# Kernel optimization log

Measured on AMD Instinct MI355X. Metric: run time of the kernel, lower is better.

Reference implementation:

```python
import jax, jax.numpy as jnp
import numpy as np

N = 50000
E = 500000
STRUCT = 128
SEM = 768
HID = 128
HEADS = 4


def setup_inputs() -> dict:
    key = jax.random.key(0)
    ks = jax.random.split(key, 16)
    rn = lambda k, s, sc=0.05: jax.random.normal(k, s, dtype=jnp.float32) * sc
    in_dim = STRUCT + SEM
    return {
        "x": rn(ks[0], (N, in_dim), 1.0),
        "edge_index": jax.random.randint(ks[1], (2, E), 0, N),
        "Wq": rn(ks[2], (STRUCT, HID)),
        "Wk": rn(ks[3], (SEM, HID)),
        "Wv": rn(ks[4], (SEM, HID)),
        "Wo": rn(ks[5], (STRUCT + HID, STRUCT)),
        "bo": jnp.zeros((STRUCT,), jnp.float32),
        "W1": rn(ks[6], (in_dim, HEADS * HID)),
        "att_src1": rn(ks[7], (HEADS, HID)),
        "att_dst1": rn(ks[8], (HEADS, HID)),
        "b1": jnp.zeros((HEADS * HID,), jnp.float32),
        "g1_w": jnp.ones((HEADS * HID,), jnp.float32),
        "g1_b": jnp.zeros((HEADS * HID,), jnp.float32),
        "g1_ms": jnp.ones((HEADS * HID,), jnp.float32),
        "W2": rn(ks[9], (HEADS * HID, HID)),
        "att_src2": rn(ks[10], (1, HID)),
        "att_dst2": rn(ks[11], (1, HID)),
        "b2": jnp.zeros((HID,), jnp.float32),
        "g2_w": jnp.ones((HID,), jnp.float32),
        "g2_b": jnp.zeros((HID,), jnp.float32),
        "g2_ms": jnp.ones((HID,), jnp.float32),
        "Wn": rn(ks[12], (HID, 2)),
        "bn": jnp.zeros((2,), jnp.float32),
    }


def gat_conv(x, src, dst, W, att_src, att_dst, bias, heads, out_c, concat):
    # PyG GATConv (self loops already appended to src/dst by caller)
    n = x.shape[0]
    h = (x @ W).reshape(n, heads, out_c)              # [N,H,C]
    a_src = (h * att_src).sum(-1)                      # [N,H]
    a_dst = (h * att_dst).sum(-1)                      # [N,H]
    alpha = jax.nn.leaky_relu(a_src[src] + a_dst[dst], 0.2)  # [Etot,H]
    amax = jax.ops.segment_max(alpha, dst, num_segments=n)
    amax = jnp.where(jnp.isfinite(amax), amax, 0.0)
    ex = jnp.exp(alpha - amax[dst])
    denom = jax.ops.segment_sum(ex, dst, num_segments=n)
    att = ex / (denom[dst] + 1e-16)                    # segment softmax over dst
    msg = h[src] * att[:, :, None]                     # [Etot,H,C]
    out = jax.ops.segment_sum(msg, dst, num_segments=n)
    out = out.reshape(n, heads * out_c) if concat else out.mean(1)
    return out + bias


def graph_norm(x, weight, bias, mean_scale, eps=1e-5):
    mean = x.mean(0, keepdims=True)
    out = x - mean * mean_scale
    var = (out * out).mean(0, keepdims=True)
    return out / jnp.sqrt(var + eps) * weight + bias


def reference(x, edge_index, Wq, Wk, Wv, Wo, bo, W1, att_src1, att_dst1, b1,
              g1_w, g1_b, g1_ms, W2, att_src2, att_dst2, b2, g2_w, g2_b, g2_ms,
              Wn, bn):
    x_struct = x[:, :STRUCT]
    x_sem = x[:, STRUCT:]
    # CrossModalFusion
    Q = x_struct @ Wq
    K = x_sem @ Wk
    V = x_sem @ Wv
    scores = (Q * K).sum(-1, keepdims=True)
    attn = jax.nn.sigmoid(scores) * V
    h0 = jnp.concatenate([x_struct, attn], axis=1) @ Wo + bo
    h = jnp.concatenate([h0, x_sem], axis=1)
    # add self loops once
    n = x.shape[0]
    loop = jnp.arange(n, dtype=edge_index.dtype)
    src = jnp.concatenate([edge_index[0], loop])
    dst = jnp.concatenate([edge_index[1], loop])
    h = gat_conv(h, src, dst, W1, att_src1, att_dst1, b1, HEADS, HID, True)
    h = jax.nn.elu(graph_norm(h, g1_w, g1_b, g1_ms))
    h = gat_conv(h, src, dst, W2, att_src2, att_dst2, b2, 1, HID, False)
    h = jax.nn.elu(graph_norm(h, g2_w, g2_b, g2_ms))
    return h @ Wn + bn
```

## Files before the change

### kernel.cpp

```cpp
#include <hip/hip_runtime.h>
#include <math.h>

#define NN 50000
#define NE 500000
#define EEDG 550000
#define SDIM 128
#define MDIM 768
#define HIDD 128
#define NHEADS 4
#define INDIM 896
#define H1D 512
#define SCAN_NB 196
#define MP 50048
#define MT 391

typedef unsigned short u16;
typedef unsigned int u32;
typedef __attribute__((ext_vector_type(8))) short short8;
typedef __attribute__((ext_vector_type(4))) float f32x4;

__device__ __forceinline__ u16 f2bf(float f) {
    union { float f; u32 u; } v; v.f = f;
    u32 r = v.u + 0x7FFFu + ((v.u >> 16) & 1u);
    return (u16)(r >> 16);
}
__device__ __forceinline__ float bf2f(u16 h) {
    union { u32 u; float f; } v; v.u = ((u32)h) << 16;
    return v.f;
}

__device__ __forceinline__ void gl_lds16(const u16* g, u16* l) {
    __builtin_amdgcn_global_load_lds(
        (const __attribute__((address_space(1))) void*)g,
        (__attribute__((address_space(3))) void*)l, 16, 0, 0);
}

__device__ __forceinline__ void edge_sd(const int* __restrict__ ei, int e, int& s, int& d) {
    if (e < NE) { s = ei[e]; d = ei[NE + e]; }
    else        { s = e - NE; d = e - NE; }
}

__global__ __launch_bounds__(256) void cast_weights(
    const float* __restrict__ Wq, const float* __restrict__ Wk, const float* __restrict__ Wv,
    const float* __restrict__ Wo, const float* __restrict__ W1, const float* __restrict__ W2,
    u16* __restrict__ wqT, u16* __restrict__ wkT, u16* __restrict__ wvT,
    u16* __restrict__ woT, u16* __restrict__ w1T, u16* __restrict__ w2T,
    int* __restrict__ degcur, float* __restrict__ msum)
{
    const int SQ = 128 * 128, SK = 128 * 768, SV = 128 * 768,
              SO = 256 * 128, S1 = 896 * 512, S2 = 512 * 128;
    long i = (long)blockIdx.x * 256 + threadIdx.x;
    long w = i;
    if (w < SQ) { int n = (int)(w / 128), k = (int)(w % 128); wqT[w] = f2bf(Wq[(size_t)k * 128 + n]); return; }
    w -= SQ;
    if (w < SK) { int n = (int)(w / 768), k = (int)(w % 768); wkT[w] = f2bf(Wk[(size_t)k * 128 + n]); return; }
    w -= SK;
    if (w < SV) { int n = (int)(w / 768), k = (int)(w % 768); wvT[w] = f2bf(Wv[(size_t)k * 128 + n]); return; }
    w -= SV;
    if (w < SO) { int n = (int)(w / 256), k = (int)(w % 256); woT[w] = f2bf(Wo[(size_t)k * 128 + n]); return; }
    w -= SO;
    if (w < S1) { int n = (int)(w / 896), k = (int)(w % 896); w1T[w] = f2bf(W1[(size_t)k * 512 + n]); return; }
    w -= S1;
    if (w < S2) { int n = (int)(w / 512), k = (int)(w % 512); w2T[w] = f2bf(W2[(size_t)k * 128 + n]); return; }
    w -= S2;
    if (w < 2 * NN) { degcur[w] = 0; return; }
    w -= 2 * NN;
    if (w < 1024) msum[w] = 0.f;
}

__global__ __launch_bounds__(256) void cast_pad_x(const float4* __restrict__ x4, u16* __restrict__ xb) {
    const long total = (long)MP * 224;
    long i = (long)blockIdx.x * blockDim.x + threadIdx.x;
    long stride = (long)gridDim.x * blockDim.x;
    for (; i < total; i += stride) {
        int row = (int)(i / 224);
        int c4 = (int)(i - (long)row * 224);
        float4 v = make_float4(0.f, 0.f, 0.f, 0.f);
        if (row < NN) v = x4[(size_t)row * 224 + c4];
        short4 o;
        o.x = (short)f2bf(v.x); o.y = (short)f2bf(v.y);
        o.z = (short)f2bf(v.z); o.w = (short)f2bf(v.w);
        *(short4*)(xb + (size_t)row * 896 + c4 * 4) = o;
    }
}

__global__ __launch_bounds__(256) void count_deg(const int* __restrict__ ei, int* __restrict__ deg) {
    int e = blockIdx.x * 256 + threadIdx.x;
    if (e >= EEDG) return;
    int d = e < NE ? ei[NE + e] : e - NE;
    atomicAdd(&deg[d], 1);
}

__global__ __launch_bounds__(256) void scan_bsum(const int* __restrict__ deg, int* __restrict__ part) {
    __shared__ int s[256];
    int t = threadIdx.x;
    int idx = blockIdx.x * 256 + t;
    s[t] = idx < NN ? deg[idx] : 0;
    __syncthreads();
    for (int off = 128; off; off >>= 1) {
        if (t < off) s[t] += s[t + off];
        __syncthreads();
    }
    if (t == 0) part[blockIdx.x] = s[0];
}

__global__ __launch_bounds__(256) void scan_part(int* __restrict__ part) {
    __shared__ int s[256];
    int t = threadIdx.x;
    int v = t < SCAN_NB ? part[t] : 0;
    s[t] = v;
    __syncthreads();
    for (int off = 1; off < 256; off <<= 1) {
        int x = t >= off ? s[t - off] : 0;
        __syncthreads();
        s[t] += x;
        __syncthreads();
    }
    if (t < SCAN_NB) part[t] = s[t] - v;
}

__global__ __launch_bounds__(256) void scan_write(const int* __restrict__ deg, const int* __restrict__ part,
                                                  int* __restrict__ rowptr) {
    __shared__ int s[256];
    int t = threadIdx.x;
    int idx = blockIdx.x * 256 + t;
    int v = idx < NN ? deg[idx] : 0;
    s[t] = v;
    __syncthreads();
    for (int off = 1; off < 256; off <<= 1) {
        int x = t >= off ? s[t - off] : 0;
        __syncthreads();
        s[t] += x;
        __syncthreads();
    }
    if (idx < NN) rowptr[idx] = part[blockIdx.x] + s[t] - v;
    if (idx == NN - 1) rowptr[NN] = EEDG;
}

__global__ __launch_bounds__(256) void fill_csr(const int* __restrict__ ei, const int* __restrict__ rowptr,
                                                int* __restrict__ cur, int* __restrict__ esrc,
                                                int* __restrict__ edst) {
    int e = blockIdx.x * 256 + threadIdx.x;
    if (e >= EEDG) return;
    int s, d;
    edge_sd(ei, e, s, d);
    int p = rowptr[d] + atomicAdd(&cur[d], 1);
    esrc[p] = s;
    edst[p] = d;
}

template<int H>
__global__ __launch_bounds__(256) void edge_exp(const int* __restrict__ esrc, const int* __restrict__ edst,
    const float* __restrict__ asrc, const float* __restrict__ adst, float* __restrict__ exf)
{
    int i = blockIdx.x * 256 + threadIdx.x;
    if (i >= EEDG) return;
    int s = esrc[i], d = edst[i];
    if (H == 4) {
        float4 as = *(const float4*)(asrc + s * 4);
        float4 ad = *(const float4*)(adst + d * 4);
        float4 o;
        float a;
        a = as.x + ad.x; a = a >= 0.f ? a : 0.2f * a; o.x = expf(a);
        a = as.y + ad.y; a = a >= 0.f ? a : 0.2f * a; o.y = expf(a);
        a = as.z + ad.z; a = a >= 0.f ? a : 0.2f * a; o.z = expf(a);
        a = as.w + ad.w; a = a >= 0.f ? a : 0.2f * a; o.w = expf(a);
        *(float4*)(exf + (size_t)i * 4) = o;
    } else {
        float a = asrc[s] + adst[d];
        a = a >= 0.f ? a : 0.2f * a;
        exf[i] = expf(a);
    }
}

template<int OUT_BF16, int DOTS, int DH>
__device__ __forceinline__ void gemm_body(
    u16* __restrict__ Asm, u16* __restrict__ Bsm,
    const u16* __restrict__ A1, int lda1, int K1,
    const u16* __restrict__ A2, int lda2, int K2,
    const u16* __restrict__ Bw,
    void* __restrict__ Cout, int ldc,
    const float* __restrict__ bias, int row0, int col0,
    const float* __restrict__ dvs, const float* __restrict__ dvd,
    float* __restrict__ aout_s, float* __restrict__ aout_d)
{
    const int tid = threadIdx.x;
    const int wave = tid >> 6, lane = tid & 63;
    const int wr = wave >> 1, wc = wave & 1;
    const int K = K1 + K2;
    const int srow = tid >> 2;
    const int skp = (tid & 3) * 8;
    const int l15 = lane & 15, l4 = lane >> 4;

    f32x4 acc[4][4];
    #pragma unroll
    for (int i = 0; i < 4; ++i)
        #pragma unroll
        for (int j = 0; j < 4; ++j)
            acc[i][j] = (f32x4){0.f, 0.f, 0.f, 0.f};

    for (int k0 = 0; k0 < K; k0 += 32) {
        const u16* Ab; int la; int kk;
        if (k0 < K1) { Ab = A1; la = lda1; kk = k0; }
        else         { Ab = A2; la = lda2; kk = k0 - K1; }
        gl_lds16(Ab + (size_t)(row0 + srow) * la + kk + skp,      Asm + srow * 32 + skp);
        gl_lds16(Ab + (size_t)(row0 + srow + 64) * la + kk + skp, Asm + (srow + 64) * 32 + skp);
        gl_lds16(Bw + (size_t)(col0 + srow) * K + k0 + skp,       Bsm + srow * 32 + skp);
        gl_lds16(Bw + (size_t)(col0 + srow + 64) * K + k0 + skp,  Bsm + (srow + 64) * 32 + skp);
        __syncthreads();
        short8 af[4], bfr[4];
        #pragma unroll
        for (int m = 0; m < 4; ++m)
            af[m] = *(const short8*)(Asm + (wr * 64 + m * 16 + l15) * 32 + l4 * 8);
        #pragma unroll
        for (int n = 0; n < 4; ++n)
            bfr[n] = *(const short8*)(Bsm + (wc * 64 + n * 16 + l15) * 32 + l4 * 8);
        #pragma unroll
        for (int m = 0; m < 4; ++m)
            #pragma unroll
            for (int n = 0; n < 4; ++n)
                acc[m][n] = __builtin_amdgcn_mfma_f32_16x16x32_bf16(af[m], bfr[n], acc[m][n], 0, 0, 0);
        __syncthreads();
    }
    #pragma unroll
    for (int m = 0; m < 4; ++m) {
        int r = row0 + wr * 64 + m * 16 + l4 * 4;
        #pragma unroll
        for (int n = 0; n < 4; ++n) {
            int c = col0 + wc * 64 + n * 16 + l15;
            float bv = bias ? bias[c] : 0.f;
            #pragma unroll
            for (int q = 0; q < 4; ++q) {
                float v = acc[m][n][q] + bv;
                if (OUT_BF16) ((u16*)Cout)[(size_t)(r + q) * ldc + c] = f2bf(v);
                else          ((float*)Cout)[(size_t)(r + q) * ldc + c] = v;
            }
        }
    }
    if (DOTS) {
        const int head = (DH == 1) ? 0 : (col0 >> 7);
        const float* svp = dvs + head * 128;
        const float* dvp = dvd + head * 128;
        float sv[4], dv[4];
        #pragma unroll
        for (int n = 0; n < 4; ++n) {
            int cc = wc * 64 + n * 16 + l15;
            sv[n] = svp[cc];
            dv[n] = dvp[cc];
        }
        __shared__ float red[128][2][2];
        #pragma unroll
        for (int m = 0; m < 4; ++m) {
            #pragma unroll
            for (int q = 0; q < 4; ++q) {
                float ps = 0.f, pd = 0.f;
                #pragma unroll
                for (int n = 0; n < 4; ++n) {
                    ps = fmaf(acc[m][n][q], sv[n], ps);
                    pd = fmaf(acc[m][n][q], dv[n], pd);
                }
                #pragma unroll
                for (int off = 1; off < 16; off <<= 1) {
                    ps += __shfl_xor(ps, off);
                    pd += __shfl_xor(pd, off);
                }
                if (l15 == 0) {
                    int lr = wr * 64 + m * 16 + l4 * 4 + q;
                    red[lr][wc][0] = ps;
                    red[lr][wc][1] = pd;
                }
            }
        }
        __syncthreads();
        if (tid < 128) {
            int r = row0 + tid;
            aout_s[(size_t)r * DH + head] = red[tid][0][0] + red[tid][1][0];
            aout_d[(size_t)r * DH + head] = red[tid][0][1] + red[tid][1][1];
        }
    }
}

template<int OUT_BF16, int DOTS, int DH>
__global__ __launch_bounds__(256) void gemm_mfma(
    const u16* __restrict__ A1, int lda1, int K1,
    const u16* __restrict__ A2, int lda2, int K2,
    const u16* __restrict__ Bw,
    void* __restrict__ Cout, int ldc,
    const float* __restrict__ bias,
    const float* __restrict__ dvs, const float* __restrict__ dvd,
    float* __restrict__ aout_s, float* __restrict__ aout_d)
{
    __shared__ u16 Asm[128 * 32];
    __shared__ u16 Bsm[128 * 32];
    gemm_body<OUT_BF16, DOTS, DH>(Asm, Bsm, A1, lda1, K1, A2, lda2, K2, Bw, Cout, ldc, bias,
                                  blockIdx.y * 128, blockIdx.x * 128, dvs, dvd, aout_s, aout_d);
}

__global__ __launch_bounds__(256) void gemm_w1(
    const u16* __restrict__ A1, const u16* __restrict__ A2,
    const u16* __restrict__ Bw, u16* __restrict__ Cout)
{
    __shared__ u16 Asm[128 * 32];
    __shared__ u16 Bsm[128 * 32];
    const int nwg = 4 * MT;
    const int q = nwg / 8, r = nwg % 8;
    int orig = blockIdx.x;
    int xcd = orig & 7;
    int lg = (xcd < r ? xcd * (q + 1) : r * (q + 1) + (xcd - r) * q) + (orig >> 3);
    int col0 = (lg & 3) * 128;
    int row0 = (lg >> 2) * 128;
    gemm_body<1, 0, 1>(Asm, Bsm, A1, 128, 128, A2, 896, 768, Bw, Cout, 512, nullptr,
                       row0, col0, nullptr, nullptr, nullptr, nullptr);
}

__global__ __launch_bounds__(256) void gemm_qkv(
    const u16* __restrict__ xb,
    const u16* __restrict__ wqT, const u16* __restrict__ wkT, const u16* __restrict__ wvT,
    u16* __restrict__ qb, u16* __restrict__ kb, u16* __restrict__ vb)
{
    __shared__ u16 Asm[128 * 32];
    __shared__ u16 Bsm[128 * 32];
    const u16* A; const u16* B; int K; u16* C;
    if (blockIdx.x == 0)      { A = xb;       B = wqT; K = 128; C = qb; }
    else if (blockIdx.x == 1) { A = xb + 128; B = wkT; K = 768; C = kb; }
    else                      { A = xb + 128; B = wvT; K = 768; C = vb; }
    gemm_body<1, 0, 1>(Asm, Bsm, A, 896, K, (const u16*)nullptr, 0, 0, B, C, 128, nullptr,
                       blockIdx.y * 128, 0, nullptr, nullptr, nullptr, nullptr);
}

__global__ __launch_bounds__(128) void node_attn_b(const u16* __restrict__ Q,
                                                   const u16* __restrict__ K,
                                                   u16* __restrict__ V)
{
    int nd = blockIdx.x;
    int t = threadIdx.x;
    size_t base = (size_t)nd * HIDD;
    float p = bf2f(Q[base + t]) * bf2f(K[base + t]);
    #pragma unroll
    for (int off = 32; off; off >>= 1) p += __shfl_down(p, off);
    __shared__ float sm[2];
    if ((t & 63) == 0) sm[t >> 6] = p;
    __syncthreads();
    float s = sm[0] + sm[1];
    float sig = 1.f / (1.f + expf(-s));
    V[base + t] = f2bf(bf2f(V[base + t]) * sig);
}

__global__ __launch_bounds__(256) void att_dots1_b(const u16* __restrict__ h1,
    const float* __restrict__ asv, const float* __restrict__ adv,
    float* __restrict__ a_src, float* __restrict__ a_dst)
{
    int nd = blockIdx.x;
    int t = threadIdx.x;
    int w = t >> 6, l = t & 63;
    const u16* hr = h1 + (size_t)nd * H1D + w * HIDD;
    const float* sv = asv + w * HIDD;
    const float* dv = adv + w * HIDD;
    float h0v = bf2f(hr[l]), h1v = bf2f(hr[l + 64]);
    float ps = h0v * sv[l] + h1v * sv[l + 64];
    float pd = h0v * dv[l] + h1v * dv[l + 64];
    #pragma unroll
    for (int off = 32; off; off >>= 1) {
        ps += __shfl_down(ps, off);
        pd += __shfl_down(pd, off);
    }
    if (l == 0) { a_src[nd * NHEADS + w] = ps; a_dst[nd * NHEADS + w] = pd; }
}

#define ACC4(P, AA) { \
    n0 = fmaf(bf2f((u16)(P).x), AA, n0); \
    n1 = fmaf(bf2f((u16)((P).x >> 16)), AA, n1); \
    n2 = fmaf(bf2f((u16)(P).y), AA, n2); \
    n3 = fmaf(bf2f((u16)((P).y >> 16)), AA, n3); }

__global__ __launch_bounds__(128) void agg1_f(const int* __restrict__ rowptr, const int* __restrict__ esrc,
    const float* __restrict__ exf,
    const u16* __restrict__ h1b, const float* __restrict__ bias, u16* __restrict__ o1b)
{
    int d = blockIdx.x;
    int t = threadIdx.x;
    int c0 = t * 4;
    int h = t >> 5;
    int beg = rowptr[d], end = rowptr[d + 1];
    float n0 = 0.f, n1 = 0.f, n2 = 0.f, n3 = 0.f, den = 0.f;
    int i = beg;
    for (; i + 7 < end; i += 8) {
        int s0 = esrc[i], s1 = esrc[i+1], s2 = esrc[i+2], s3 = esrc[i+3];
        int s4 = esrc[i+4], s5 = esrc[i+5], s6 = esrc[i+6], s7 = esrc[i+7];
        float a0 = exf[(size_t)i*4+h],     a1 = exf[(size_t)(i+1)*4+h];
        float a2 = exf[(size_t)(i+2)*4+h], a3 = exf[(size_t)(i+3)*4+h];
        float a4 = exf[(size_t)(i+4)*4+h], a5 = exf[(size_t)(i+5)*4+h];
        float a6 = exf[(size_t)(i+6)*4+h], a7 = exf[(size_t)(i+7)*4+h];
        uint2 p0 = *(const uint2*)(h1b + (size_t)s0 * H1D + c0);
        uint2 p1 = *(const uint2*)(h1b + (size_t)s1 * H1D + c0);
        uint2 p2 = *(const uint2*)(h1b + (size_t)s2 * H1D + c0);
        uint2 p3 = *(const uint2*)(h1b + (size_t)s3 * H1D + c0);
        uint2 p4 = *(const uint2*)(h1b + (size_t)s4 * H1D + c0);
        uint2 p5 = *(const uint2*)(h1b + (size_t)s5 * H1D + c0);
        uint2 p6 = *(const uint2*)(h1b + (size_t)s6 * H1D + c0);
        uint2 p7 = *(const uint2*)(h1b + (size_t)s7 * H1D + c0);
        den += ((a0 + a1) + (a2 + a3)) + ((a4 + a5) + (a6 + a7));
        ACC4(p0, a0) ACC4(p1, a1) ACC4(p2, a2) ACC4(p3, a3)
        ACC4(p4, a4) ACC4(p5, a5) ACC4(p6, a6) ACC4(p7, a7)
    }
    for (; i < end; ++i) {
        int sA = esrc[i];
        float aA = exf[(size_t)i * 4 + h];
        uint2 pA = *(const uint2*)(h1b + (size_t)sA * H1D + c0);
        den += aA;
        ACC4(pA, aA)
    }
    float invd = 1.f / (den + 1e-16f);
    float4 bv = *(const float4*)(bias + c0);
    u32 o0 = (u32)f2bf(n0 * invd + bv.x) | ((u32)f2bf(n1 * invd + bv.y) << 16);
    u32 o1 = (u32)f2bf(n2 * invd + bv.z) | ((u32)f2bf(n3 * invd + bv.w) << 16);
    *(uint2*)(o1b + (size_t)d * H1D + c0) = make_uint2(o0, o1);
}

__global__ __launch_bounds__(256) void agg2_f(const int* __restrict__ rowptr, const int* __restrict__ esrc,
    const float* __restrict__ exf,
    const u16* __restrict__ h2b, const float* __restrict__ bias, float* __restrict__ o2,
    float* __restrict__ msum)
{
    if (blockIdx.x == 0) {
        msum[threadIdx.x] = 0.f;
        msum[threadIdx.x + 256] = 0.f;
        msum[threadIdx.x + 512] = 0.f;
        msum[threadIdx.x + 768] = 0.f;
    }
    int w = threadIdx.x >> 6, l = threadIdx.x & 63;
    int d = blockIdx.x * 4 + w;
    if (d >= NN) return;
    int c0 = l * 2;
    int beg = rowptr[d], end = rowptr[d + 1];
    float n0 = 0.f, n1 = 0.f, den = 0.f;
    int i = beg;
    for (; i + 7 < end; i += 8) {
        int s0 = esrc[i], s1 = esrc[i+1], s2 = esrc[i+2], s3 = esrc[i+3];
        int s4 = esrc[i+4], s5 = esrc[i+5], s6 = esrc[i+6], s7 = esrc[i+7];
        float a0 = exf[i],   a1 = exf[i+1], a2 = exf[i+2], a3 = exf[i+3];
        float a4 = exf[i+4], a5 = exf[i+5], a6 = exf[i+6], a7 = exf[i+7];
        u32 p0 = *(const u32*)(h2b + (size_t)s0 * HIDD + c0);
        u32 p1 = *(const u32*)(h2b + (size_t)s1 * HIDD + c0);
        u32 p2 = *(const u32*)(h2b + (size_t)s2 * HIDD + c0);
        u32 p3 = *(const u32*)(h2b + (size_t)s3 * HIDD + c0);
        u32 p4 = *(const u32*)(h2b + (size_t)s4 * HIDD + c0);
        u32 p5 = *(const u32*)(h2b + (size_t)s5 * HIDD + c0);
        u32 p6 = *(const u32*)(h2b + (size_t)s6 * HIDD + c0);
        u32 p7 = *(const u32*)(h2b + (size_t)s7 * HIDD + c0);
        den += ((a0 + a1) + (a2 + a3)) + ((a4 + a5) + (a6 + a7));
        n0 = fmaf(bf2f((u16)p0), a0, n0); n1 = fmaf(bf2f((u16)(p0 >> 16)), a0, n1);
        n0 = fmaf(bf2f((u16)p1), a1, n0); n1 = fmaf(bf2f((u16)(p1 >> 16)), a1, n1);
        n0 = fmaf(bf2f((u16)p2), a2, n0); n1 = fmaf(bf2f((u16)(p2 >> 16)), a2, n1);
        n0 = fmaf(bf2f((u16)p3), a3, n0); n1 = fmaf(bf2f((u16)(p3 >> 16)), a3, n1);
        n0 = fmaf(bf2f((u16)p4), a4, n0); n1 = fmaf(bf2f((u16)(p4 >> 16)), a4, n1);
        n0 = fmaf(bf2f((u16)p5), a5, n0); n1 = fmaf(bf2f((u16)(p5 >> 16)), a5, n1);
        n0 = fmaf(bf2f((u16)p6), a6, n0); n1 = fmaf(bf2f((u16)(p6 >> 16)), a6, n1);
        n0 = fmaf(bf2f((u16)p7), a7, n0); n1 = fmaf(bf2f((u16)(p7 >> 16)), a7, n1);
    }
    for (; i < end; ++i) {
        int sA = esrc[i];
        float aA = exf[i];
        u32 pA = *(const u32*)(h2b + (size_t)sA * HIDD + c0);
        den += aA;
        n0 = fmaf(bf2f((u16)pA), aA, n0);
        n1 = fmaf(bf2f((u16)(pA >> 16)), aA, n1);
    }
    float invd = 1.f / (den + 1e-16f);
    o2[(size_t)d * HIDD + c0]     = n0 * invd + bias[c0];
    o2[(size_t)d * HIDD + c0 + 1] = n1 * invd + bias[c0 + 1];
}

__global__ void colstat_b(const u16* __restrict__ x, float* __restrict__ msum,
                          float* __restrict__ vsum, int n, int rpb)
{
    int C = blockDim.x;
    int c = threadIdx.x;
    int r0 = blockIdx.x * rpb;
    int r1 = min(n, r0 + rpb);
    float s = 0.f, s2 = 0.f;
    for (int r = r0; r < r1; ++r) {
        float v = bf2f(x[(size_t)r * C + c]);
        s += v;
        s2 += v * v;
    }
    atomicAdd(&msum[c], s);
    atomicAdd(&vsum[c], s2);
}

__global__ void apply_norm_elu_b(u16* __restrict__ x, const float* __restrict__ msum,
                                 const float* __restrict__ vsum, const float* __restrict__ ms,
                                 const float* __restrict__ w, const float* __restrict__ b,
                                 int n, int rpb)
{
    int C = blockDim.x;
    int c = threadIdx.x;
    const float invn = 1.f / (float)NN;
    float mean = msum[c] * invn;
    float sub = mean * ms[c];
    float var = vsum[c] * invn - 2.f * sub * mean + sub * sub;
    float inv = rsqrtf(var + 1e-5f);
    float wc = w[c] * inv, bc = b[c];
    int r0 = blockIdx.x * rpb;
    int r1 = min(n, r0 + rpb);
    for (int r = r0; r < r1; ++r) {
        float v = (bf2f(x[(size_t)r * C + c]) - sub) * wc + bc;
        v = v > 0.f ? v : expm1f(v);
        x[(size_t)r * C + c] = f2bf(v);
    }
}

__global__ void colstat(const float* __restrict__ x, float* __restrict__ msum,
                        float* __restrict__ vsum, int n, int rpb)
{
    int C = blockDim.x;
    int c = threadIdx.x;
    int r0 = blockIdx.x * rpb;
    int r1 = min(n, r0 + rpb);
    float s = 0.f, s2 = 0.f;
    for (int r = r0; r < r1; ++r) {
        float v = x[(size_t)r * C + c];
        s += v;
        s2 += v * v;
    }
    atomicAdd(&msum[c], s);
    atomicAdd(&vsum[c], s2);
}

__global__ __launch_bounds__(128) void norm2_proj(const float* __restrict__ o2,
    const float* __restrict__ msum, const float* __restrict__ vsum,
    const float* __restrict__ ms, const float* __restrict__ w, const float* __restrict__ b,
    const float* __restrict__ Wn, const float* __restrict__ bn, float* __restrict__ out)
{
    int nd = blockIdx.x;
    int t = threadIdx.x;
    const float invn = 1.f / (float)NN;
    float mean = msum[t] * invn;
    float sub = mean * ms[t];
    float var = vsum[t] * invn - 2.f * sub * mean + sub * sub;
    float inv = rsqrtf(var + 1e-5f);
    float v = (o2[(size_t)nd * HIDD + t] - sub) * w[t] * inv + b[t];
    v = v > 0.f ? v : expm1f(v);
    float p0 = v * Wn[t * 2], p1 = v * Wn[t * 2 + 1];
    #pragma unroll
    for (int off = 32; off; off >>= 1) {
        p0 += __shfl_down(p0, off);
        p1 += __shfl_down(p1, off);
    }
    __shared__ float sm[4];
    if ((t & 63) == 0) { sm[t >> 6] = p0; sm[2 + (t >> 6)] = p1; }
    __syncthreads();
    if (t == 0) {
        out[nd * 2 + 0] = sm[0] + sm[1] + bn[0];
        out[nd * 2 + 1] = sm[2] + sm[3] + bn[1];
    }
}

extern "C" void kernel_launch(void* const* d_in, const int* in_sizes, int n_in,
                              void* d_out, int out_size, void* d_ws, size_t ws_size,
                              hipStream_t stream)
{
    const float* x   = (const float*)d_in[0];
    const int*   ei  = (const int*)d_in[1];
    const float* Wq  = (const float*)d_in[2];
    const float* Wk  = (const float*)d_in[3];
    const float* Wv  = (const float*)d_in[4];
    const float* Wo  = (const float*)d_in[5];
    const float* bo  = (const float*)d_in[6];
    const float* W1  = (const float*)d_in[7];
    const float* as1 = (const float*)d_in[8];
    const float* ad1 = (const float*)d_in[9];
    const float* b1  = (const float*)d_in[10];
    const float* g1w = (const float*)d_in[11];
    const float* g1b = (const float*)d_in[12];
    const float* g1m = (const float*)d_in[13];
    const float* W2  = (const float*)d_in[14];
    const float* as2 = (const float*)d_in[15];
    const float* ad2 = (const float*)d_in[16];
    const float* b2  = (const float*)d_in[17];
    const float* g2w = (const float*)d_in[18];
    const float* g2b = (const float*)d_in[19];
    const float* g2m = (const float*)d_in[20];
    const float* Wn  = (const float*)d_in[21];
    const float* bn  = (const float*)d_in[22];
    float* out = (float*)d_out;

    u16* usw = (u16*)d_ws;
    size_t uo = 0;
    u16* xb  = usw + uo; uo += (size_t)MP * 896;
    u16* h1b = usw + uo; uo += (size_t)MP * 512;
    u16* qb  = usw + uo; uo += (size_t)MP * 128;
    u16* kb  = usw + uo; uo += (size_t)MP * 128;
    u16* vb  = usw + uo; uo += (size_t)MP * 128;
    u16* o1b = usw + uo; uo += (size_t)MP * 512;
    u16* wqT = usw + uo; uo += 128 * 128;
    u16* wkT = usw + uo; uo += 128 * 768;
    u16* wvT = usw + uo; uo += 128 * 768;
    u16* woT = usw + uo; uo += 128 * 256;
    u16* w1T = usw + uo; uo += 512 * 896;
    u16* w2T = usw + uo; uo += 128 * 512;
    float* fws = (float*)(usw + uo);
    size_t fo = 0;
    float* asrc = fws + fo; fo += (size_t)MP * NHEADS;
    float* adst = fws + fo; fo += (size_t)MP * NHEADS;
    float* exf  = fws + fo; fo += (size_t)EEDG * NHEADS;
    float* msum = fws + fo; fo += 512;
    float* vsum = fws + fo; fo += 512;
    int* iws = (int*)(fws + fo);
    size_t io = 0;
    int* rowptr = iws + io; io += NN + 1;
    int* degcur = iws + io; io += 2 * NN;
    int* esrc   = iws + io; io += EEDG;
    int* edst   = iws + io; io += EEDG;
    int* spart  = iws + io; io += 256;
    int* cur    = degcur + NN;
    float* o2  = (float*)xb;
    u16* h0b = qb;
    u16* h2b = kb;

    const int EB = (EEDG + 255) / 256;
    const int CW_BLOCKS = (770048 + 2 * NN + 1024 + 255) / 256;

    cast_weights<<<CW_BLOCKS, 256, 0, stream>>>(Wq, Wk, Wv, Wo, W1, W2,
                                                wqT, wkT, wvT, woT, w1T, w2T,
                                                degcur, msum);
    cast_pad_x<<<8192, 256, 0, stream>>>((const float4*)x, xb);

    count_deg<<<EB, 256, 0, stream>>>(ei, degcur);
    scan_bsum<<<SCAN_NB, 256, 0, stream>>>(degcur, spart);
    scan_part<<<1, 256, 0, stream>>>(spart);
    scan_write<<<SCAN_NB, 256, 0, stream>>>(degcur, spart, rowptr);
    fill_csr<<<EB, 256, 0, stream>>>(ei, rowptr, cur, esrc, edst);

    gemm_qkv<<<dim3(3, MT), 256, 0, stream>>>(xb, wqT, wkT, wvT, qb, kb, vb);
    node_attn_b<<<NN, 128, 0, stream>>>(qb, kb, vb);

    gemm_mfma<1, 0, 1><<<dim3(1, MT), 256, 0, stream>>>(xb, 896, 128, vb, 128, 128, woT, h0b, 128, bo,
                                                        nullptr, nullptr, nullptr, nullptr);

    gemm_w1<<<4 * MT, 256, 0, stream>>>(h0b, xb + 128, w1T, h1b);

    att_dots1_b<<<NN, 256, 0, stream>>>(h1b, as1, ad1, asrc, adst);
    edge_exp<NHEADS><<<EB, 256, 0, stream>>>(esrc, edst, asrc, adst, exf);
    agg1_f<<<NN, 128, 0, stream>>>(rowptr, esrc, exf, h1b, b1, o1b);

    colstat_b<<<(NN + 127) / 128, H1D, 0, stream>>>(o1b, msum, vsum, NN, 128);
    apply_norm_elu_b<<<(NN + 127) / 128, H1D, 0, stream>>>(o1b, msum, vsum, g1m, g1w, g1b, NN, 128);

    gemm_mfma<1, 1, 1><<<dim3(1, MT), 256, 0, stream>>>(o1b, 512, 512, (const u16*)nullptr, 0, 0, w2T, h2b, 128,
                                                        nullptr, as2, ad2, asrc, adst);
    edge_exp<1><<<EB, 256, 0, stream>>>(esrc, edst, asrc, adst, exf);
    agg2_f<<<(NN + 3) / 4, 256, 0, stream>>>(rowptr, esrc, exf, h2b, b2, o2, msum);

    colstat<<<(NN + 127) / 128, HIDD, 0, stream>>>(o2, msum, vsum, NN, 128);
    norm2_proj<<<NN, 128, 0, stream>>>(o2, msum, vsum, g2m, g2w, g2b, Wn, bn, out);
}
```

Baseline: 608.4 us.

## Merge independent prep kernels and fuse layer-1 column stats into aggregation

Degree counting is merged into the x-cast launch, and CSR fill is merged into the QKV GEMM launch as extra blocks. This removes launches and lets independent work overlap. The separate colstat pass over o1b is removed: agg1_f now accumulates column sums and squared sums with atomics into 32 partitioned buffers, and the normalization kernel reduces those partitions. This saves a full read of the 50000x512 activation, but adds 4M float atomics with contention across 32 partitions.

```diff
diff --git a/kernel.cpp b/kernel.cpp
--- a/kernel.cpp
+++ b/kernel.cpp
@@ -13,6 +13,8 @@
 #define SCAN_NB 196
 #define MP 50048
 #define MT 391
+#define EB 2149
+#define NPART 32
 
 typedef unsigned short u16;
 typedef unsigned int u32;
@@ -65,13 +67,22 @@
     w -= S2;
     if (w < 2 * NN) { degcur[w] = 0; return; }
     w -= 2 * NN;
-    if (w < 1024) msum[w] = 0.f;
-}
-
-__global__ __launch_bounds__(256) void cast_pad_x(const float4* __restrict__ x4, u16* __restrict__ xb) {
+    if (w < 1024 + 2 * NPART * 512) msum[w] = 0.f;
+}
+
+__global__ __launch_bounds__(256) void prep2(const int* __restrict__ ei, int* __restrict__ deg,
+                                             const float4* __restrict__ x4, u16* __restrict__ xb)
+{
+    if (blockIdx.x < EB) {
+        int e = blockIdx.x * 256 + threadIdx.x;
+        if (e >= EEDG) return;
+        int d = e < NE ? ei[NE + e] : e - NE;
+        atomicAdd(&deg[d], 1);
+        return;
+    }
     const long total = (long)MP * 224;
-    long i = (long)blockIdx.x * blockDim.x + threadIdx.x;
-    long stride = (long)gridDim.x * blockDim.x;
+    long i = (long)(blockIdx.x - EB) * 256 + threadIdx.x;
+    long stride = (long)(gridDim.x - EB) * 256;
     for (; i < total; i += stride) {
         int row = (int)(i / 224);
         int c4 = (int)(i - (long)row * 224);
@@ -82,13 +93,6 @@
         o.z = (short)f2bf(v.z); o.w = (short)f2bf(v.w);
         *(short4*)(xb + (size_t)row * 896 + c4 * 4) = o;
     }
-}
-
-__global__ __launch_bounds__(256) void count_deg(const int* __restrict__ ei, int* __restrict__ deg) {
-    int e = blockIdx.x * 256 + threadIdx.x;
-    if (e >= EEDG) return;
-    int d = e < NE ? ei[NE + e] : e - NE;
-    atomicAdd(&deg[d], 1);
 }
 
 __global__ __launch_bounds__(256) void scan_bsum(const int* __restrict__ deg, int* __restrict__ part) {
@@ -135,18 +139,6 @@
     }
     if (idx < NN) rowptr[idx] = part[blockIdx.x] + s[t] - v;
     if (idx == NN - 1) rowptr[NN] = EEDG;
-}
-
-__global__ __launch_bounds__(256) void fill_csr(const int* __restrict__ ei, const int* __restrict__ rowptr,
-                                                int* __restrict__ cur, int* __restrict__ esrc,
-                                                int* __restrict__ edst) {
-    int e = blockIdx.x * 256 + threadIdx.x;
-    if (e >= EEDG) return;
-    int s, d;
-    edge_sd(ei, e, s, d);
-    int p = rowptr[d] + atomicAdd(&cur[d], 1);
-    esrc[p] = s;
-    edst[p] = d;
 }
 
 template<int H>
@@ -313,19 +305,34 @@
                        row0, col0, nullptr, nullptr, nullptr, nullptr);
 }
 
-__global__ __launch_bounds__(256) void gemm_qkv(
+__global__ __launch_bounds__(256) void gemm_qkv_fill(
     const u16* __restrict__ xb,
     const u16* __restrict__ wqT, const u16* __restrict__ wkT, const u16* __restrict__ wvT,
-    u16* __restrict__ qb, u16* __restrict__ kb, u16* __restrict__ vb)
+    u16* __restrict__ qb, u16* __restrict__ kb, u16* __restrict__ vb,
+    const int* __restrict__ ei, const int* __restrict__ rowptr,
+    int* __restrict__ cur, int* __restrict__ esrc, int* __restrict__ edst)
 {
     __shared__ u16 Asm[128 * 32];
     __shared__ u16 Bsm[128 * 32];
+    int bid = blockIdx.x;
+    if (bid >= 3 * MT) {
+        int e = (bid - 3 * MT) * 256 + threadIdx.x;
+        if (e >= EEDG) return;
+        int s, d;
+        edge_sd(ei, e, s, d);
+        int p = rowptr[d] + atomicAdd(&cur[d], 1);
+        esrc[p] = s;
+        edst[p] = d;
+        return;
+    }
+    int sel = bid / MT;
+    int row = bid - sel * MT;
     const u16* A; const u16* B; int K; u16* C;
-    if (blockIdx.x == 0)      { A = xb;       B = wqT; K = 128; C = qb; }
-    else if (blockIdx.x == 1) { A = xb + 128; B = wkT; K = 768; C = kb; }
-    else                      { A = xb + 128; B = wvT; K = 768; C = vb; }
+    if (sel == 0)      { A = xb;       B = wqT; K = 128; C = qb; }
+    else if (sel == 1) { A = xb + 128; B = wkT; K = 768; C = kb; }
+    else               { A = xb + 128; B = wvT; K = 768; C = vb; }
     gemm_body<1, 0, 1>(Asm, Bsm, A, 896, K, (const u16*)nullptr, 0, 0, B, C, 128, nullptr,
-                       blockIdx.y * 128, 0, nullptr, nullptr, nullptr, nullptr);
+                       row * 128, 0, nullptr, nullptr, nullptr, nullptr);
 }
 
 __global__ __launch_bounds__(128) void node_attn_b(const u16* __restrict__ Q,
@@ -375,7 +382,8 @@
 
 __global__ __launch_bounds__(128) void agg1_f(const int* __restrict__ rowptr, const int* __restrict__ esrc,
     const float* __restrict__ exf,
-    const u16* __restrict__ h1b, const float* __restrict__ bias, u16* __restrict__ o1b)
+    const u16* __restrict__ h1b, const float* __restrict__ bias, u16* __restrict__ o1b,
+    float* __restrict__ statm, float* __restrict__ statv)
 {
     int d = blockIdx.x;
     int t = threadIdx.x;
@@ -412,9 +420,19 @@
     }
     float invd = 1.f / (den + 1e-16f);
     float4 bv = *(const float4*)(bias + c0);
-    u32 o0 = (u32)f2bf(n0 * invd + bv.x) | ((u32)f2bf(n1 * invd + bv.y) << 16);
-    u32 o1 = (u32)f2bf(n2 * invd + bv.z) | ((u32)f2bf(n3 * invd + bv.w) << 16);
-    *(uint2*)(o1b + (size_t)d * H1D + c0) = make_uint2(o0, o1);
+    u16 q0 = f2bf(n0 * invd + bv.x);
+    u16 q1 = f2bf(n1 * invd + bv.y);
+    u16 q2 = f2bf(n2 * invd + bv.z);
+    u16 q3 = f2bf(n3 * invd + bv.w);
+    *(uint2*)(o1b + (size_t)d * H1D + c0) =
+        make_uint2((u32)q0 | ((u32)q1 << 16), (u32)q2 | ((u32)q3 << 16));
+    float r0 = bf2f(q0), r1 = bf2f(q1), r2 = bf2f(q2), r3 = bf2f(q3);
+    float* sm_ = statm + (d & (NPART - 1)) * 512 + c0;
+    float* sv_ = statv + (d & (NPART - 1)) * 512 + c0;
+    atomicAdd(sm_ + 0, r0); atomicAdd(sv_ + 0, r0 * r0);
+    atomicAdd(sm_ + 1, r1); atomicAdd(sv_ + 1, r1 * r1);
+    atomicAdd(sm_ + 2, r2); atomicAdd(sv_ + 2, r2 * r2);
+    atomicAdd(sm_ + 3, r3); atomicAdd(sv_ + 3, r3 * r3);
 }
 
 __global__ __launch_bounds__(256) void agg2_f(const int* __restrict__ rowptr, const int* __restrict__ esrc,
@@ -471,34 +489,23 @@
     o2[(size_t)d * HIDD + c0 + 1] = n1 * invd + bias[c0 + 1];
 }
 
-__global__ void colstat_b(const u16* __restrict__ x, float* __restrict__ msum,
-                          float* __restrict__ vsum, int n, int rpb)
+__global__ void apply_norm_elu_b(u16* __restrict__ x, const float* __restrict__ statm,
+                                 const float* __restrict__ statv, const float* __restrict__ ms,
+                                 const float* __restrict__ w, const float* __restrict__ b,
+                                 int n, int rpb)
 {
     int C = blockDim.x;
     int c = threadIdx.x;
-    int r0 = blockIdx.x * rpb;
-    int r1 = min(n, r0 + rpb);
-    float s = 0.f, s2 = 0.f;
-    for (int r = r0; r < r1; ++r) {
-        float v = bf2f(x[(size_t)r * C + c]);
-        s += v;
-        s2 += v * v;
-    }
-    atomicAdd(&msum[c], s);
-    atomicAdd(&vsum[c], s2);
-}
-
-__global__ void apply_norm_elu_b(u16* __restrict__ x, const float* __restrict__ msum,
-                                 const float* __restrict__ vsum, const float* __restrict__ ms,
-                                 const float* __restrict__ w, const float* __restrict__ b,
-                                 int n, int rpb)
-{
-    int C = blockDim.x;
-    int c = threadIdx.x;
+    float msum_ = 0.f, vsum_ = 0.f;
+    #pragma unroll
+    for (int p = 0; p < NPART; ++p) {
+        msum_ += statm[p * 512 + c];
+        vsum_ += statv[p * 512 + c];
+    }
     const float invn = 1.f / (float)NN;
-    float mean = msum[c] * invn;
+    float mean = msum_ * invn;
     float sub = mean * ms[c];
-    float var = vsum[c] * invn - 2.f * sub * mean + sub * sub;
+    float var = vsum_ * invn - 2.f * sub * mean + sub * sub;
     float inv = rsqrtf(var + 1e-5f);
     float wc = w[c] * inv, bc = b[c];
     int r0 = blockIdx.x * rpb;
@@ -606,6 +613,8 @@
     float* exf  = fws + fo; fo += (size_t)EEDG * NHEADS;
     float* msum = fws + fo; fo += 512;
     float* vsum = fws + fo; fo += 512;
+    float* statm = fws + fo; fo += NPART * 512;
+    float* statv = fws + fo; fo += NPART * 512;
     int* iws = (int*)(fws + fo);
     size_t io = 0;
     int* rowptr = iws + io; io += NN + 1;
@@ -618,21 +627,19 @@
     u16* h0b = qb;
     u16* h2b = kb;
 
-    const int EB = (EEDG + 255) / 256;
-    const int CW_BLOCKS = (770048 + 2 * NN + 1024 + 255) / 256;
+    const int CW_BLOCKS = (770048 + 2 * NN + 1024 + 2 * NPART * 512 + 255) / 256;
 
     cast_weights<<<CW_BLOCKS, 256, 0, stream>>>(Wq, Wk, Wv, Wo, W1, W2,
                                                 wqT, wkT, wvT, woT, w1T, w2T,
                                                 degcur, msum);
-    cast_pad_x<<<8192, 256, 0, stream>>>((const float4*)x, xb);
-
-    count_deg<<<EB, 256, 0, stream>>>(ei, degcur);
+    prep2<<<EB + 8192, 256, 0, stream>>>(ei, degcur, (const float4*)x, xb);
+
     scan_bsum<<<SCAN_NB, 256, 0, stream>>>(degcur, spart);
     scan_part<<<1, 256, 0, stream>>>(spart);
     scan_write<<<SCAN_NB, 256, 0, stream>>>(degcur, spart, rowptr);
-    fill_csr<<<EB, 256, 0, stream>>>(ei, rowptr, cur, esrc, edst);
-
-    gemm_qkv<<<dim3(3, MT), 256, 0, stream>>>(xb, wqT, wkT, wvT, qb, kb, vb);
+
+    gemm_qkv_fill<<<3 * MT + EB, 256, 0, stream>>>(xb, wqT, wkT, wvT, qb, kb, vb,
+                                                   ei, rowptr, cur, esrc, edst);
     node_attn_b<<<NN, 128, 0, stream>>>(qb, kb, vb);
 
     gemm_mfma<1, 0, 1><<<dim3(1, MT), 256, 0, stream>>>(xb, 896, 128, vb, 128, 128, woT, h0b, 128, bo,
@@ -642,10 +649,9 @@
 
     att_dots1_b<<<NN, 256, 0, stream>>>(h1b, as1, ad1, asrc, adst);
     edge_exp<NHEADS><<<EB, 256, 0, stream>>>(esrc, edst, asrc, adst, exf);
-    agg1_f<<<NN, 128, 0, stream>>>(rowptr, esrc, exf, h1b, b1, o1b);
-
-    colstat_b<<<(NN + 127) / 128, H1D, 0, stream>>>(o1b, msum, vsum, NN, 128);
-    apply_norm_elu_b<<<(NN + 127) / 128, H1D, 0, stream>>>(o1b, msum, vsum, g1m, g1w, g1b, NN, 128);
+    agg1_f<<<NN, 128, 0, stream>>>(rowptr, esrc, exf, h1b, b1, o1b, statm, statv);
+
+    apply_norm_elu_b<<<(NN + 127) / 128, H1D, 0, stream>>>(o1b, statm, statv, g1m, g1w, g1b, NN, 128);
 
     gemm_mfma<1, 1, 1><<<dim3(1, MT), 256, 0, stream>>>(o1b, 512, 512, (const u16*)nullptr, 0, 0, w2T, h2b, 128,
                                                         nullptr, as2, ad2, asrc, adst);
```

Measured after the change: 1.265 ms. 2.08x slower.

## Merge independent graph-prep kernels into GEMM/cast launches to overlap work

Applied to the files above, without the earlier changes.

Folds degree counting into the x-cast kernel and CSR fill into the QKV GEMM kernel using block-index partitioning, so independent graph-building work runs concurrently with dense work and two launches are removed. The QKV grid also changes from 2D (3 x MT) to 1D with a sel/row decode. This is meant to hide the small, latency-bound atomic kernels behind the larger bandwidth/compute kernels. The cost is that the fill blocks allocate unused LDS, and the mixed block types may unbalance scheduling.

```diff
diff --git a/kernel.cpp b/kernel.cpp
--- a/kernel.cpp
+++ b/kernel.cpp
@@ -13,6 +13,7 @@
 #define SCAN_NB 196
 #define MP 50048
 #define MT 391
+#define EB 2149
 
 typedef unsigned short u16;
 typedef unsigned int u32;
@@ -68,10 +69,19 @@
     if (w < 1024) msum[w] = 0.f;
 }
 
-__global__ __launch_bounds__(256) void cast_pad_x(const float4* __restrict__ x4, u16* __restrict__ xb) {
+__global__ __launch_bounds__(256) void prep2(const int* __restrict__ ei, int* __restrict__ deg,
+                                             const float4* __restrict__ x4, u16* __restrict__ xb)
+{
+    if (blockIdx.x < EB) {
+        int e = blockIdx.x * 256 + threadIdx.x;
+        if (e >= EEDG) return;
+        int d = e < NE ? ei[NE + e] : e - NE;
+        atomicAdd(&deg[d], 1);
+        return;
+    }
     const long total = (long)MP * 224;
-    long i = (long)blockIdx.x * blockDim.x + threadIdx.x;
-    long stride = (long)gridDim.x * blockDim.x;
+    long i = (long)(blockIdx.x - EB) * 256 + threadIdx.x;
+    long stride = (long)(gridDim.x - EB) * 256;
     for (; i < total; i += stride) {
         int row = (int)(i / 224);
         int c4 = (int)(i - (long)row * 224);
@@ -82,13 +92,6 @@
         o.z = (short)f2bf(v.z); o.w = (short)f2bf(v.w);
         *(short4*)(xb + (size_t)row * 896 + c4 * 4) = o;
     }
-}
-
-__global__ __launch_bounds__(256) void count_deg(const int* __restrict__ ei, int* __restrict__ deg) {
-    int e = blockIdx.x * 256 + threadIdx.x;
-    if (e >= EEDG) return;
-    int d = e < NE ? ei[NE + e] : e - NE;
-    atomicAdd(&deg[d], 1);
 }
 
 __global__ __launch_bounds__(256) void scan_bsum(const int* __restrict__ deg, int* __restrict__ part) {
@@ -135,18 +138,6 @@
     }
     if (idx < NN) rowptr[idx] = part[blockIdx.x] + s[t] - v;
     if (idx == NN - 1) rowptr[NN] = EEDG;
-}
-
-__global__ __launch_bounds__(256) void fill_csr(const int* __restrict__ ei, const int* __restrict__ rowptr,
-                                                int* __restrict__ cur, int* __restrict__ esrc,
-                                                int* __restrict__ edst) {
-    int e = blockIdx.x * 256 + threadIdx.x;
-    if (e >= EEDG) return;
-    int s, d;
-    edge_sd(ei, e, s, d);
-    int p = rowptr[d] + atomicAdd(&cur[d], 1);
-    esrc[p] = s;
-    edst[p] = d;
 }
 
 template<int H>
@@ -313,19 +304,34 @@
                        row0, col0, nullptr, nullptr, nullptr, nullptr);
 }
 
-__global__ __launch_bounds__(256) void gemm_qkv(
+__global__ __launch_bounds__(256) void gemm_qkv_fill(
     const u16* __restrict__ xb,
     const u16* __restrict__ wqT, const u16* __restrict__ wkT, const u16* __restrict__ wvT,
-    u16* __restrict__ qb, u16* __restrict__ kb, u16* __restrict__ vb)
+    u16* __restrict__ qb, u16* __restrict__ kb, u16* __restrict__ vb,
+    const int* __restrict__ ei, const int* __restrict__ rowptr,
+    int* __restrict__ cur, int* __restrict__ esrc, int* __restrict__ edst)
 {
     __shared__ u16 Asm[128 * 32];
     __shared__ u16 Bsm[128 * 32];
+    int bid = blockIdx.x;
+    if (bid >= 3 * MT) {
+        int e = (bid - 3 * MT) * 256 + threadIdx.x;
+        if (e >= EEDG) return;
+        int s, d;
+        edge_sd(ei, e, s, d);
+        int p = rowptr[d] + atomicAdd(&cur[d], 1);
+        esrc[p] = s;
+        edst[p] = d;
+        return;
+    }
+    int sel = bid / MT;
+    int row = bid - sel * MT;
     const u16* A; const u16* B; int K; u16* C;
-    if (blockIdx.x == 0)      { A = xb;       B = wqT; K = 128; C = qb; }
-    else if (blockIdx.x == 1) { A = xb + 128; B = wkT; K = 768; C = kb; }
-    else                      { A = xb + 128; B = wvT; K = 768; C = vb; }
+    if (sel == 0)      { A = xb;       B = wqT; K = 128; C = qb; }
+    else if (sel == 1) { A = xb + 128; B = wkT; K = 768; C = kb; }
+    else               { A = xb + 128; B = wvT; K = 768; C = vb; }
     gemm_body<1, 0, 1>(Asm, Bsm, A, 896, K, (const u16*)nullptr, 0, 0, B, C, 128, nullptr,
-                       blockIdx.y * 128, 0, nullptr, nullptr, nullptr, nullptr);
+                       row * 128, 0, nullptr, nullptr, nullptr, nullptr);
 }
 
 __global__ __launch_bounds__(128) void node_attn_b(const u16* __restrict__ Q,
@@ -618,21 +624,19 @@
     u16* h0b = qb;
     u16* h2b = kb;
 
-    const int EB = (EEDG + 255) / 256;
     const int CW_BLOCKS = (770048 + 2 * NN + 1024 + 255) / 256;
 
     cast_weights<<<CW_BLOCKS, 256, 0, stream>>>(Wq, Wk, Wv, Wo, W1, W2,
                                                 wqT, wkT, wvT, woT, w1T, w2T,
                                                 degcur, msum);
-    cast_pad_x<<<8192, 256, 0, stream>>>((const float4*)x, xb);
-
-    count_deg<<<EB, 256, 0, stream>>>(ei, degcur);
+    prep2<<<EB + 8192, 256, 0, stream>>>(ei, degcur, (const float4*)x, xb);
+
     scan_bsum<<<SCAN_NB, 256, 0, stream>>>(degcur, spart);
     scan_part<<<1, 256, 0, stream>>>(spart);
     scan_write<<<SCAN_NB, 256, 0, stream>>>(degcur, spart, rowptr);
-    fill_csr<<<EB, 256, 0, stream>>>(ei, rowptr, cur, esrc, edst);
-
-    gemm_qkv<<<dim3(3, MT), 256, 0, stream>>>(xb, wqT, wkT, wvT, qb, kb, vb);
+
+    gemm_qkv_fill<<<3 * MT + EB, 256, 0, stream>>>(xb, wqT, wkT, wvT, qb, kb, vb,
+                                                   ei, rowptr, cur, esrc, edst);
     node_attn_b<<<NN, 128, 0, stream>>>(qb, kb, vb);
 
     gemm_mfma<1, 0, 1><<<dim3(1, MT), 256, 0, stream>>>(xb, 896, 128, vb, 128, 128, woT, h0b, 128, bo,
```

Measured after the change: 590.7 us. 2.9% less time.
